# Optimization experiments

Measured on AMD Instinct MI355X. Metric: run time of the kernel, lower is better.

The kernel has to match this reference:

```python
import jax, jax.numpy as jnp
import numpy as np

BS, V, C, A = 8, 4096, 64, 12   # batch, vertices, channels, anchors (anchor_size=12 hardcoded in source)
K = 4                            # neighbor_num
POOLING_RATE = 4
POOL = V // POOLING_RATE


def setup_inputs() -> dict:
    key = jax.random.key(0)
    k1, k2, k3 = jax.random.split(key, 3)
    vertices = jax.random.normal(k1, (BS, V, 3), dtype=jnp.float32)
    feature_map = jax.random.normal(k2, (BS, C, V, A), dtype=jnp.float32)
    # deterministic stand-in for torch.randperm(V)[:POOL]
    sample_idx = jax.random.permutation(k3, V)[:POOL].astype(jnp.int32)
    return {"vertices": vertices, "feature_map": feature_map, "sample_idx": sample_idx}


def reference(vertices, feature_map, sample_idx):
    bs, v, _ = vertices.shape
    c, a = feature_map.shape[1], feature_map.shape[3]
    k = K
    # pairwise squared euclidean distances: (bs, v, v)
    inner = jnp.einsum('bic,bjc->bij', vertices, vertices)
    quad = jnp.sum(vertices * vertices, axis=2)                     # (bs, v)
    dist = -2.0 * inner + quad[:, None, :] + quad[:, :, None]
    # k+1 smallest, drop self (first entry)
    _, idx = jax.lax.top_k(-dist, k + 1)                            # (bs, v, k+1)
    nbr = idx[:, :, 1:]                                             # (bs, v, k)
    # gather neighbor features along vertex axis (axis=2 of feature_map)
    idx_b = jnp.broadcast_to(nbr.reshape(bs, 1, v * k, 1), (bs, c, v * k, a))
    nbr_feat = jnp.take_along_axis(feature_map, idx_b, axis=2)      # (bs, c, v*k, a)
    nbr_feat = nbr_feat.reshape(bs, c, v, k, a)
    pooled = jnp.max(nbr_feat, axis=3)                              # (bs, c, v, a)
    vertices_pool = vertices[:, sample_idx, :]                      # (bs, pool, 3)
    feature_map_pool = pooled[:, :, sample_idx, :]                  # (bs, c, pool, a)
    return vertices_pool, feature_map_pool
```

## Files before the change

### kernel.cpp

```cpp
#include <hip/hip_runtime.h>
#include <stdint.h>

#define BS 8
#define V 4096
#define C 64
#define A 12
#define KNB 4
#define POOL 1024
#define CC 512
#define NCC (V / CC)
#define QPB 256
#define NQC (POOL / QPB)

__global__ __launch_bounds__(256) void knn_chunk_kernel(
    const float* __restrict__ vtx,
    const int* __restrict__ sidx,
    unsigned long long* __restrict__ partial)
{
    __shared__ float4 cand[CC];

    const int bid = blockIdx.x;
    const int cc = bid % NCC;
    const int qc = (bid / NCC) % NQC;
    const int b  = bid / (NCC * NQC);
    const int tid = threadIdx.x;

    const float* vb = vtx + (size_t)b * V * 3;

    for (int t = tid; t < CC; t += 256) {
        const int j = cc * CC + t;
        const float x = vb[j * 3 + 0];
        const float y = vb[j * 3 + 1];
        const float z = vb[j * 3 + 2];
        float q;
        {
#pragma clang fp contract(off)
            q = (x * x + y * y) + z * z;
        }
        cand[t] = make_float4(x, y, z, q);
    }
    __syncthreads();

    const int s = qc * QPB + tid;
    const int gq = sidx[s];
    const float qx = vb[gq * 3 + 0];
    const float qy = vb[gq * 3 + 1];
    const float qz = vb[gq * 3 + 2];
    float qq;
    {
#pragma clang fp contract(off)
        qq = (qx * qx + qy * qy) + qz * qz;
    }

    unsigned long long k0 = ~0ull, k1 = ~0ull, k2 = ~0ull, k3 = ~0ull, k4 = ~0ull;

#pragma unroll 8
    for (int jj = 0; jj < CC; ++jj) {
        const float4 cd = cand[jj];
        const float inner = fmaf(cd.z, qz, fmaf(cd.y, qy, cd.x * qx));
        const float d = fmaf(-2.0f, inner, cd.w) + qq;
        const unsigned int bits = __float_as_uint(d);
        const unsigned int msk = (unsigned int)(((int)bits) >> 31) | 0x80000000u;
        const unsigned int u = bits ^ msk;
        const unsigned long long key =
            ((unsigned long long)u << 32) | (unsigned int)(cc * CC + jj);
        if (key < k4) {
            k4 = key;
            if (k4 < k3) { unsigned long long t = k3; k3 = k4; k4 = t; }
            if (k3 < k2) { unsigned long long t = k2; k2 = k3; k3 = t; }
            if (k2 < k1) { unsigned long long t = k1; k1 = k2; k2 = t; }
            if (k1 < k0) { unsigned long long t = k0; k0 = k1; k1 = t; }
        }
    }

    const size_t off = ((size_t)(b * POOL + s) * NCC + cc) * 5;
    partial[off + 0] = k0;
    partial[off + 1] = k1;
    partial[off + 2] = k2;
    partial[off + 3] = k3;
    partial[off + 4] = k4;
}

__global__ __launch_bounds__(256) void knn_merge_kernel(
    const unsigned long long* __restrict__ partial,
    const float* __restrict__ vtx,
    const int* __restrict__ sidx,
    int* __restrict__ nbr,
    float* __restrict__ outv)
{
    const int t = blockIdx.x * 256 + threadIdx.x;
    if (t >= BS * POOL) return;
    const int b = t / POOL;
    const int s = t % POOL;

    const unsigned long long* p = partial + (size_t)t * (NCC * 5);
    unsigned long long k0 = ~0ull, k1 = ~0ull, k2 = ~0ull, k3 = ~0ull, k4 = ~0ull;
#pragma unroll
    for (int i = 0; i < NCC * 5; ++i) {
        const unsigned long long key = p[i];
        if (key < k4) {
            k4 = key;
            if (k4 < k3) { unsigned long long tt = k3; k3 = k4; k4 = tt; }
            if (k3 < k2) { unsigned long long tt = k2; k2 = k3; k3 = tt; }
            if (k2 < k1) { unsigned long long tt = k1; k1 = k2; k2 = tt; }
            if (k1 < k0) { unsigned long long tt = k0; k0 = k1; k1 = tt; }
        }
    }
    int4 nb;
    nb.x = (int)(unsigned int)k1;
    nb.y = (int)(unsigned int)k2;
    nb.z = (int)(unsigned int)k3;
    nb.w = (int)(unsigned int)k4;
    ((int4*)nbr)[t] = nb;

    const int gq = sidx[s];
    const float* vv = vtx + ((size_t)b * V + gq) * 3;
    outv[(size_t)t * 3 + 0] = vv[0];
    outv[(size_t)t * 3 + 1] = vv[1];
    outv[(size_t)t * 3 + 2] = vv[2];
}

__device__ inline float4 f4max(float4 a, float4 b) {
    return make_float4(fmaxf(a.x, b.x), fmaxf(a.y, b.y),
                       fmaxf(a.z, b.z), fmaxf(a.w, b.w));
}

__global__ __launch_bounds__(256) void gather_pool_kernel(
    const float* __restrict__ fm,
    const int* __restrict__ nbr,
    float* __restrict__ outf)
{
    const int t = blockIdx.x * 256 + threadIdx.x;
    const int s = t % POOL;
    const int c = (t / POOL) % C;
    const int b = t / (POOL * C);

    const int4 nb = ((const int4*)nbr)[b * POOL + s];

    const float4* base = (const float4*)fm + (size_t)(b * C + c) * V * 3;

    float4 r0 = base[(size_t)nb.x * 3 + 0];
    float4 r1 = base[(size_t)nb.x * 3 + 1];
    float4 r2 = base[(size_t)nb.x * 3 + 2];

    float4 s0 = base[(size_t)nb.y * 3 + 0];
    float4 s1 = base[(size_t)nb.y * 3 + 1];
    float4 s2 = base[(size_t)nb.y * 3 + 2];
    r0 = f4max(r0, s0); r1 = f4max(r1, s1); r2 = f4max(r2, s2);

    s0 = base[(size_t)nb.z * 3 + 0];
    s1 = base[(size_t)nb.z * 3 + 1];
    s2 = base[(size_t)nb.z * 3 + 2];
    r0 = f4max(r0, s0); r1 = f4max(r1, s1); r2 = f4max(r2, s2);

    s0 = base[(size_t)nb.w * 3 + 0];
    s1 = base[(size_t)nb.w * 3 + 1];
    s2 = base[(size_t)nb.w * 3 + 2];
    r0 = f4max(r0, s0); r1 = f4max(r1, s1); r2 = f4max(r2, s2);

    float4* dst = (float4*)outf + (size_t)t * 3;
    dst[0] = r0;
    dst[1] = r1;
    dst[2] = r2;
}

extern "C" void kernel_launch(void* const* d_in, const int* in_sizes, int n_in,
                              void* d_out, int out_size, void* d_ws, size_t ws_size,
                              hipStream_t stream) {
    const float* vtx = (const float*)d_in[0];
    const float* fm  = (const float*)d_in[1];
    const int* sidx  = (const int*)d_in[2];
    float* out = (float*)d_out;

    unsigned long long* partial = (unsigned long long*)d_ws;
    const size_t partial_bytes = (size_t)BS * POOL * NCC * 5 * sizeof(unsigned long long);
    int* nbr = (int*)((char*)d_ws + partial_bytes);

    float* outv = out;
    float* outf = out + (size_t)BS * POOL * 3;

    knn_chunk_kernel<<<BS * NQC * NCC, 256, 0, stream>>>(vtx, sidx, partial);
    knn_merge_kernel<<<(BS * POOL) / 256, 256, 0, stream>>>(partial, vtx, sidx, nbr, outv);
    gather_pool_kernel<<<(BS * C * POOL) / 256, 256, 0, stream>>>(fm, nbr, outf);
}
```

Baseline: 270.4 us.

## Split KNN candidate chunks finer and use 32-bit branchless top-5 insertion

Raises the number of candidate chunks from 8 to 32 (or 16 if the workspace is small), so the KNN chunk kernel launches many more blocks and fills the GPU better. The per-thread top-5 list now holds separate 32-bit distance and index arrays, updated with branchless selects instead of 64-bit compare-swap chains. The merge kernel skips a whole chunk when that chunk's best entry cannot enter the list. In exchange, each thread writes more partial results and the merge reads more data, with a workspace-size dependent path.

```diff
diff --git a/kernel.cpp b/kernel.cpp
--- a/kernel.cpp
+++ b/kernel.cpp
@@ -5,24 +5,21 @@
 #define V 4096
 #define C 64
 #define A 12
-#define KNB 4
 #define POOL 1024
-#define CC 512
-#define NCC (V / CC)
-#define QPB 256
-#define NQC (POOL / QPB)
-
+
+template<int NCC>
 __global__ __launch_bounds__(256) void knn_chunk_kernel(
     const float* __restrict__ vtx,
     const int* __restrict__ sidx,
     unsigned long long* __restrict__ partial)
 {
+    constexpr int CC = V / NCC;
     __shared__ float4 cand[CC];
 
     const int bid = blockIdx.x;
     const int cc = bid % NCC;
-    const int qc = (bid / NCC) % NQC;
-    const int b  = bid / (NCC * NQC);
+    const int qc = (bid / NCC) & 3;
+    const int b  = bid / (NCC * 4);
     const int tid = threadIdx.x;
 
     const float* vb = vtx + (size_t)b * V * 3;
@@ -41,7 +38,7 @@
     }
     __syncthreads();
 
-    const int s = qc * QPB + tid;
+    const int s = qc * 256 + tid;
     const int gq = sidx[s];
     const float qx = vb[gq * 3 + 0];
     const float qy = vb[gq * 3 + 1];
@@ -52,7 +49,8 @@
         qq = (qx * qx + qy * qy) + qz * qz;
     }
 
-    unsigned long long k0 = ~0ull, k1 = ~0ull, k2 = ~0ull, k3 = ~0ull, k4 = ~0ull;
+    unsigned int h0 = ~0u, h1 = ~0u, h2 = ~0u, h3 = ~0u, h4 = ~0u;
+    unsigned int l0 = 0, l1 = 0, l2 = 0, l3 = 0, l4 = 0;
 
 #pragma unroll 8
     for (int jj = 0; jj < CC; ++jj) {
@@ -60,27 +58,27 @@
         const float inner = fmaf(cd.z, qz, fmaf(cd.y, qy, cd.x * qx));
         const float d = fmaf(-2.0f, inner, cd.w) + qq;
         const unsigned int bits = __float_as_uint(d);
-        const unsigned int msk = (unsigned int)(((int)bits) >> 31) | 0x80000000u;
-        const unsigned int u = bits ^ msk;
-        const unsigned long long key =
-            ((unsigned long long)u << 32) | (unsigned int)(cc * CC + jj);
-        if (key < k4) {
-            k4 = key;
-            if (k4 < k3) { unsigned long long t = k3; k3 = k4; k4 = t; }
-            if (k3 < k2) { unsigned long long t = k2; k2 = k3; k3 = t; }
-            if (k2 < k1) { unsigned long long t = k1; k1 = k2; k2 = t; }
-            if (k1 < k0) { unsigned long long t = k0; k0 = k1; k1 = t; }
+        const unsigned int u = bits ^ ((unsigned int)(((int)bits) >> 31) | 0x80000000u);
+        const unsigned int idx = (unsigned int)(cc * CC + jj);
+        if (u < h4) {
+            const bool c0 = u < h0, c1 = u < h1, c2 = u < h2, c3 = u < h3;
+            h4 = c3 ? h3 : u;              l4 = c3 ? l3 : idx;
+            h3 = c3 ? (c2 ? h2 : u) : h3;  l3 = c3 ? (c2 ? l2 : idx) : l3;
+            h2 = c2 ? (c1 ? h1 : u) : h2;  l2 = c2 ? (c1 ? l1 : idx) : l2;
+            h1 = c1 ? (c0 ? h0 : u) : h1;  l1 = c1 ? (c0 ? l0 : idx) : l1;
+            h0 = c0 ? u : h0;              l0 = c0 ? idx : l0;
         }
     }
 
-    const size_t off = ((size_t)(b * POOL + s) * NCC + cc) * 5;
-    partial[off + 0] = k0;
-    partial[off + 1] = k1;
-    partial[off + 2] = k2;
-    partial[off + 3] = k3;
-    partial[off + 4] = k4;
-}
-
+    unsigned long long* p = partial + ((size_t)(b * POOL + s) * NCC + cc) * 5;
+    p[0] = ((unsigned long long)h0 << 32) | l0;
+    p[1] = ((unsigned long long)h1 << 32) | l1;
+    p[2] = ((unsigned long long)h2 << 32) | l2;
+    p[3] = ((unsigned long long)h3 << 32) | l3;
+    p[4] = ((unsigned long long)h4 << 32) | l4;
+}
+
+template<int NCC>
 __global__ __launch_bounds__(256) void knn_merge_kernel(
     const unsigned long long* __restrict__ partial,
     const float* __restrict__ vtx,
@@ -89,28 +87,49 @@
     float* __restrict__ outv)
 {
     const int t = blockIdx.x * 256 + threadIdx.x;
-    if (t >= BS * POOL) return;
     const int b = t / POOL;
     const int s = t % POOL;
 
     const unsigned long long* p = partial + (size_t)t * (NCC * 5);
-    unsigned long long k0 = ~0ull, k1 = ~0ull, k2 = ~0ull, k3 = ~0ull, k4 = ~0ull;
-#pragma unroll
-    for (int i = 0; i < NCC * 5; ++i) {
-        const unsigned long long key = p[i];
-        if (key < k4) {
-            k4 = key;
-            if (k4 < k3) { unsigned long long tt = k3; k3 = k4; k4 = tt; }
-            if (k3 < k2) { unsigned long long tt = k2; k2 = k3; k3 = tt; }
-            if (k2 < k1) { unsigned long long tt = k1; k1 = k2; k2 = tt; }
-            if (k1 < k0) { unsigned long long tt = k0; k0 = k1; k1 = tt; }
+
+    unsigned int h0 = ~0u, h1 = ~0u, h2 = ~0u, h3 = ~0u, h4 = ~0u;
+    unsigned int l0 = 0, l1 = 0, l2 = 0, l3 = 0, l4 = 0;
+
+#pragma unroll 4
+    for (int ccc = 0; ccc < NCC; ++ccc) {
+        const unsigned long long a0 = p[ccc * 5 + 0];
+        const unsigned long long a1 = p[ccc * 5 + 1];
+        const unsigned long long a2 = p[ccc * 5 + 2];
+        const unsigned long long a3 = p[ccc * 5 + 3];
+        const unsigned long long a4 = p[ccc * 5 + 4];
+        if ((unsigned int)(a0 >> 32) < h4) {
+#define INS(K)                                                               \
+            {                                                                \
+                const unsigned int u = (unsigned int)((K) >> 32);            \
+                const unsigned int idx = (unsigned int)(K);                  \
+                const bool c0 = u < h0, c1 = u < h1, c2 = u < h2,            \
+                           c3 = u < h3, c4 = u < h4;                         \
+                h4 = c4 ? (c3 ? h3 : u) : h4;                                \
+                l4 = c4 ? (c3 ? l3 : idx) : l4;                              \
+                h3 = c3 ? (c2 ? h2 : u) : h3;                                \
+                l3 = c3 ? (c2 ? l2 : idx) : l3;                              \
+                h2 = c2 ? (c1 ? h1 : u) : h2;                                \
+                l2 = c2 ? (c1 ? l1 : idx) : l2;                              \
+                h1 = c1 ? (c0 ? h0 : u) : h1;                                \
+                l1 = c1 ? (c0 ? l0 : idx) : l1;                              \
+                h0 = c0 ? u : h0;                                            \
+                l0 = c0 ? idx : l0;                                          \
+            }
+            INS(a0) INS(a1) INS(a2) INS(a3) INS(a4)
+#undef INS
         }
     }
+
     int4 nb;
-    nb.x = (int)(unsigned int)k1;
-    nb.y = (int)(unsigned int)k2;
-    nb.z = (int)(unsigned int)k3;
-    nb.w = (int)(unsigned int)k4;
+    nb.x = (int)l1;
+    nb.y = (int)l2;
+    nb.z = (int)l3;
+    nb.w = (int)l4;
     ((int4*)nbr)[t] = nb;
 
     const int gq = sidx[s];
@@ -172,14 +191,24 @@
     const int* sidx  = (const int*)d_in[2];
     float* out = (float*)d_out;
 
-    unsigned long long* partial = (unsigned long long*)d_ws;
-    const size_t partial_bytes = (size_t)BS * POOL * NCC * 5 * sizeof(unsigned long long);
-    int* nbr = (int*)((char*)d_ws + partial_bytes);
-
     float* outv = out;
     float* outf = out + (size_t)BS * POOL * 3;
 
-    knn_chunk_kernel<<<BS * NQC * NCC, 256, 0, stream>>>(vtx, sidx, partial);
-    knn_merge_kernel<<<(BS * POOL) / 256, 256, 0, stream>>>(partial, vtx, sidx, nbr, outv);
-    gather_pool_kernel<<<(BS * C * POOL) / 256, 256, 0, stream>>>(fm, nbr, outf);
-}
+    unsigned long long* partial = (unsigned long long*)d_ws;
+
+    const size_t need32 = (size_t)BS * POOL * 32 * 5 * 8 + (size_t)BS * POOL * 16;
+
+    if (ws_size >= need32) {
+        constexpr int NCC = 32;
+        int* nbr = (int*)((char*)d_ws + (size_t)BS * POOL * NCC * 5 * 8);
+        knn_chunk_kernel<NCC><<<BS * 4 * NCC, 256, 0, stream>>>(vtx, sidx, partial);
+        knn_merge_kernel<NCC><<<(BS * POOL) / 256, 256, 0, stream>>>(partial, vtx, sidx, nbr, outv);
+        gather_pool_kernel<<<(BS * C * POOL) / 256, 256, 0, stream>>>(fm, nbr, outf);
+    } else {
+        constexpr int NCC = 16;
+        int* nbr = (int*)((char*)d_ws + (size_t)BS * POOL * NCC * 5 * 8);
+        knn_chunk_kernel<NCC><<<BS * 4 * NCC, 256, 0, stream>>>(vtx, sidx, partial);
+        knn_merge_kernel<NCC><<<(BS * POOL) / 256, 256, 0, stream>>>(partial, vtx, sidx, nbr, outv);
+        gather_pool_kernel<<<(BS * C * POOL) / 256, 256, 0, stream>>>(fm, nbr, outf);
+    }
+}
```

New measurement: 225.7 us. 16.5% less time.
